# Kernel optimization log

Hardware: AMD Instinct MI355X
Metric: run time of the kernel (lower is better)

Reference implementation:

```python
import jax, jax.numpy as jnp
import numpy as np

SLOPE = 0.01  # torch LeakyReLU default negative_slope

def lrelu(x):
    return jax.nn.leaky_relu(x, SLOPE)

def rgcn_conv(x, edge_index, edge_type, rel_w, root_w, bias, num_relations=2):
    # PyG RGCNConv: out = x @ root + bias + sum_r mean_{edges of rel r into i}(x_j @ W_r)
    N = x.shape[0]
    src, dst = edge_index[0], edge_index[1]
    out = x @ root_w + bias
    # transform once per relation at node level, then gather per edge
    h = jnp.einsum('nd,rde->rne', x, rel_w)          # [R, N, d]
    msg = h[edge_type, src]                           # [E, d] single gather
    for r in range(num_relations):
        m = (edge_type == r)
        s = jax.ops.segment_sum(jnp.where(m[:, None], msg, 0.0), dst, num_segments=N)
        cnt = jax.ops.segment_sum(m.astype(x.dtype), dst, num_segments=N)
        out = out + s / jnp.maximum(cnt, 1.0)[:, None]  # mean aggregation (0 if no edges)
    return out


def setup_inputs() -> dict:
    key = jax.random.key(0)
    ks = jax.random.split(key, 24)
    N, E, H = 50000, 800000, 256
    Q = H // 4
    def lin(k, i, o):
        k1, k2 = jax.random.split(k)
        s = 1.0 / np.sqrt(i)
        return (jax.random.uniform(k1, (i, o), jnp.float32, -s, s),
                jax.random.uniform(k2, (o,), jnp.float32, -s, s))
    Wd, bd = lin(ks[0], 768, Q)
    Wt, bt = lin(ks[1], 768, Q)
    Wn, bn = lin(ks[2], 5, Q)
    Wc, bc = lin(ks[3], 3, Q)
    Wi, bi = lin(ks[4], H, H)
    Wo1, bo1 = lin(ks[5], H, H)
    Wo2, bo2 = lin(ks[6], H, 2)
    s = 1.0 / np.sqrt(H)
    rel_w1 = jax.random.uniform(ks[7], (2, H, H), jnp.float32, -s, s)
    root_w1 = jax.random.uniform(ks[8], (H, H), jnp.float32, -s, s)
    bias1 = jnp.zeros((H,), jnp.float32)
    rel_w2 = jax.random.uniform(ks[9], (2, H, H), jnp.float32, -s, s)
    root_w2 = jax.random.uniform(ks[10], (H, H), jnp.float32, -s, s)
    bias2 = jnp.zeros((H,), jnp.float32)
    return {
        'des': jax.random.normal(ks[11], (N, 768), jnp.float32),
        'tweet': jax.random.normal(ks[12], (N, 768), jnp.float32),
        'num_prop': jax.random.normal(ks[13], (N, 5), jnp.float32),
        'cat_prop': jax.random.normal(ks[14], (N, 3), jnp.float32),
        'edge_index': jax.random.randint(ks[15], (2, E), 0, N, jnp.int32),
        'edge_type': jax.random.randint(ks[16], (E,), 0, 2, jnp.int32),
        'Wd': Wd, 'bd': bd, 'Wt': Wt, 'bt': bt, 'Wn': Wn, 'bn': bn, 'Wc': Wc, 'bc': bc,
        'Wi': Wi, 'bi': bi,
        'rel_w1': rel_w1, 'root_w1': root_w1, 'bias1': bias1,
        'rel_w2': rel_w2, 'root_w2': root_w2, 'bias2': bias2,
        'Wo1': Wo1, 'bo1': bo1, 'Wo2': Wo2, 'bo2': bo2,
    }


def reference(des, tweet, num_prop, cat_prop, edge_index, edge_type,
              Wd, bd, Wt, bt, Wn, bn, Wc, bc, Wi, bi,
              rel_w1, root_w1, bias1, rel_w2, root_w2, bias2,
              Wo1, bo1, Wo2, bo2):
    # dropout is identity in eval mode
    d = lrelu(des @ Wd + bd)
    t = lrelu(tweet @ Wt + bt)
    n = lrelu(num_prop @ Wn + bn)
    c = lrelu(cat_prop @ Wc + bc)
    x = jnp.concatenate([d, t, n, c], axis=1)           # [N, H]
    x = lrelu(x @ Wi + bi)
    x = rgcn_conv(x, edge_index, edge_type, rel_w1, root_w1, bias1)
    x = rgcn_conv(x, edge_index, edge_type, rel_w2, root_w2, bias2)
    x = lrelu(x @ Wo1 + bo1)
    return x @ Wo2 + bo2                                 # [N, 2]
```

## Files before the change

### kernel.cpp

```cpp
#include <hip/hip_runtime.h>
#include <stdint.h>

__device__ __forceinline__ float bf2f(unsigned short h) {
    union { unsigned int u; float f; } x;
    x.u = ((unsigned int)h) << 16;
    return x.f;
}
__device__ __forceinline__ unsigned short f2bf(float f) {
    union { float f; unsigned int u; } x;
    x.f = f;
    unsigned int u = x.u;
    unsigned int r = (u + 0x7FFFu + ((u >> 16) & 1u)) >> 16;
    return (unsigned short)r;
}
__device__ __forceinline__ unsigned pk2(float a, float b) {
    unsigned ua = __float_as_uint(a) + 0x8000u;
    unsigned ub = __float_as_uint(b) + 0x8000u;
    return __builtin_amdgcn_perm(ub, ua, 0x07060302);
}

typedef __attribute__((ext_vector_type(8))) short short8;
typedef __attribute__((ext_vector_type(4))) float floatx4;

__global__ __launch_bounds__(512) void k_encode(
    const float* __restrict__ Ades, const float* __restrict__ Atw,
    const unsigned short* __restrict__ BtDes, const unsigned short* __restrict__ BtTw,
    const unsigned short* __restrict__ bias_bf,
    unsigned short* __restrict__ C, int M)
{
    __shared__ unsigned short Bs[64 * 392];
    const int set = blockIdx.y;
    const float* A = set ? Atw : Ades;
    const unsigned short* Bt = set ? BtTw : BtDes;
    const unsigned short* bias = bias_bf + set * 64;
    const int colofs = set * 64;
    const int tid  = threadIdx.x;
    const int wave = tid >> 6, lane = tid & 63;
    const int quad = lane >> 4, l16 = lane & 15;
    const int ngroups = (M + 15) >> 4;

    const int g0 = blockIdx.x * 8 + wave;
    const int g1 = g0 + (int)(gridDim.x * 8);
    const bool h1 = g1 < ngroups;
    int r0 = g0 * 16 + l16; if (r0 > M - 1) r0 = M - 1;
    int r1g = h1 ? g1 * 16 + l16 : r0; if (r1g > M - 1) r1g = M - 1;

    floatx4 acc0[4], acc1[4];
#pragma unroll
    for (int t = 0; t < 4; t++) {
        acc0[t] = (floatx4){0.f, 0.f, 0.f, 0.f};
        acc1[t] = (floatx4){0.f, 0.f, 0.f, 0.f};
    }

    const bool act0 = g0 < ngroups;

#pragma unroll
    for (int h = 0; h < 2; h++) {
        if (h) __syncthreads();
        for (int c = tid; c < 3072; c += 512) {
            int n = c / 48, kc = (c - n * 48) * 8;
            *(uint4*)&Bs[n * 392 + kc] = ((const uint4*)Bt)[n * 96 + h * 48 + (c - n * 48)];
        }
        __syncthreads();
        if (!act0) continue;

        const float* a0 = A + (size_t)r0 * 768 + h * 384 + quad * 8;
        const float* a1 = A + (size_t)r1g * 768 + h * 384 + quad * 8;
        float4 c0a = *(const float4*)(a0);
        float4 c0b = *(const float4*)(a0 + 4);
        float4 c1a = *(const float4*)(a1);
        float4 c1b = *(const float4*)(a1 + 4);
        float4 n0a = *(const float4*)(a0 + 32);
        float4 n0b = *(const float4*)(a0 + 36);
        float4 n1a = *(const float4*)(a1 + 32);
        float4 n1b = *(const float4*)(a1 + 36);

        for (int s = 0; s < 12; s++) {
            short8 af0, af1;
            unsigned* u0 = (unsigned*)&af0;
            unsigned* u1 = (unsigned*)&af1;
            u0[0] = pk2(c0a.x, c0a.y); u0[1] = pk2(c0a.z, c0a.w);
            u0[2] = pk2(c0b.x, c0b.y); u0[3] = pk2(c0b.z, c0b.w);
            u1[0] = pk2(c1a.x, c1a.y); u1[1] = pk2(c1a.z, c1a.w);
            u1[2] = pk2(c1b.x, c1b.y); u1[3] = pk2(c1b.z, c1b.w);
            c0a = n0a; c0b = n0b; c1a = n1a; c1b = n1b;
            if (s < 10) {
                n0a = *(const float4*)(a0 + (s + 2) * 32);
                n0b = *(const float4*)(a0 + (s + 2) * 32 + 4);
                n1a = *(const float4*)(a1 + (s + 2) * 32);
                n1b = *(const float4*)(a1 + (s + 2) * 32 + 4);
            }
            int kb = s * 32 + quad * 8;
#pragma unroll
            for (int t = 0; t < 4; t++) {
                short8 bfr = *(const short8*)&Bs[(t * 16 + l16) * 392 + kb];
                acc0[t] = __builtin_amdgcn_mfma_f32_16x16x32_bf16(af0, bfr, acc0[t], 0, 0, 0);
                acc1[t] = __builtin_amdgcn_mfma_f32_16x16x32_bf16(af1, bfr, acc1[t], 0, 0, 0);
            }
        }
    }

    if (act0) {
#pragma unroll
        for (int t = 0; t < 4; t++) {
            float bv = bf2f(bias[t * 16 + l16]);
#pragma unroll
            for (int r = 0; r < 4; r++) {
                int row = g0 * 16 + quad * 4 + r;
                if (row < M) {
                    float v = acc0[t][r] + bv;
                    v = v > 0.f ? v : 0.01f * v;
                    C[(size_t)row * 256 + colofs + t * 16 + l16] = f2bf(v);
                }
                if (h1) {
                    int rw = g1 * 16 + quad * 4 + r;
                    if (rw < M) {
                        float v = acc1[t][r] + bv;
                        v = v > 0.f ? v : 0.01f * v;
                        C[(size_t)rw * 256 + colofs + t * 16 + l16] = f2bf(v);
                    }
                }
            }
        }
    }
}

__global__ __launch_bounds__(256) void gemm_nt(
    const unsigned short* __restrict__ A0, const unsigned short* __restrict__ A1,
    const unsigned short* __restrict__ A2, int lda,
    const unsigned short* __restrict__ Bt, int ldb,
    unsigned short* __restrict__ C, int ldc,
    const unsigned short* __restrict__ bias,
    int M, int K, int act)
{
    constexpr int BM = 128, BN = 128, BK = 64;
    const int tid  = threadIdx.x;
    const int wave = tid >> 6;
    const int lane = tid & 63;
    const int quad = lane >> 4;
    const int l16  = lane & 15;
    const int m0   = blockIdx.x * BM;
    const int n0   = blockIdx.y * BN;
    const int wm   = (wave & 1) * 64;
    const int wn   = (wave >> 1) * 64;

    __shared__ short8 As[8 * (BM + 2)];
    __shared__ short8 Bs[8 * (BN + 2)];

    floatx4 acc[4][4];
#pragma unroll
    for (int i = 0; i < 4; i++)
#pragma unroll
        for (int j = 0; j < 4; j++) acc[i][j] = (floatx4){0.f, 0.f, 0.f, 0.f};

    for (int kt = 0; kt < K; kt += BK) {
        const unsigned short* Ap = (kt < 256) ? A0 : (kt < 512) ? A1 : A2;
        const int ko = kt & 255;
#pragma unroll
        for (int c = 0; c < 4; c++) {
            int lin = c * 256 + tid;
            int row = lin >> 3, kq = lin & 7;
            int gr = m0 + row; if (gr > M - 1) gr = M - 1;
            As[kq * (BM + 2) + row] = *(const short8*)(Ap + (size_t)gr * lda + ko + kq * 8);
        }
#pragma unroll
        for (int c = 0; c < 4; c++) {
            int lin = c * 256 + tid;
            int n = lin >> 3, kq = lin & 7;
            Bs[kq * (BN + 2) + n] = *(const short8*)(Bt + (size_t)(n0 + n) * ldb + kt + kq * 8);
        }
        __syncthreads();
#pragma unroll
        for (int s = 0; s < 2; s++) {
            short8 af[4], bfr[4];
#pragma unroll
            for (int i = 0; i < 4; i++)
                af[i] = As[(s * 4 + quad) * (BM + 2) + wm + i * 16 + l16];
#pragma unroll
            for (int j = 0; j < 4; j++)
                bfr[j] = Bs[(s * 4 + quad) * (BN + 2) + wn + j * 16 + l16];
#pragma unroll
            for (int i = 0; i < 4; i++)
#pragma unroll
                for (int j = 0; j < 4; j++)
                    acc[i][j] = __builtin_amdgcn_mfma_f32_16x16x32_bf16(
                        af[i], bfr[j], acc[i][j], 0, 0, 0);
        }
        __syncthreads();
    }

#pragma unroll
    for (int j = 0; j < 4; j++) {
        int gc = n0 + wn + j * 16 + l16;
        float bv = bias ? bf2f(bias[gc]) : 0.f;
#pragma unroll
        for (int i = 0; i < 4; i++) {
            int grb = m0 + wm + i * 16 + quad * 4;
#pragma unroll
            for (int r = 0; r < 4; r++) {
                int gr = grb + r;
                if (gr < M) {
                    float v = acc[i][j][r] + bv;
                    if (act) v = v > 0.f ? v : 0.01f * v;
                    C[(size_t)gr * ldc + gc] = f2bf(v);
                }
            }
        }
    }
}

__global__ void k_prep(const float* __restrict__ Wd, const float* __restrict__ Wt,
                       const float* __restrict__ Wi, const float* __restrict__ Wo1,
                       const float* __restrict__ root1, const float* __restrict__ rel1,
                       const float* __restrict__ root2, const float* __restrict__ rel2,
                       const float* __restrict__ bd, const float* __restrict__ bt,
                       const float* __restrict__ bi, const float* __restrict__ b1,
                       const float* __restrict__ b2, const float* __restrict__ bo1,
                       unsigned short* __restrict__ WdT, unsigned short* __restrict__ WtT,
                       unsigned short* __restrict__ WiT, unsigned short* __restrict__ Wo1T,
                       unsigned short* __restrict__ BT1, unsigned short* __restrict__ BT2,
                       unsigned short* __restrict__ bias_bf)
{
    int i = blockIdx.x * 256 + threadIdx.x;
    if (i < 49152) { int r = i >> 6, c = i & 63; WdT[c * 768 + r] = f2bf(Wd[i]); return; }
    i -= 49152;
    if (i < 49152) { int r = i >> 6, c = i & 63; WtT[c * 768 + r] = f2bf(Wt[i]); return; }
    i -= 49152;
    if (i < 65536) { int r = i >> 8, c = i & 255; WiT[c * 256 + r] = f2bf(Wi[i]); return; }
    i -= 65536;
    if (i < 65536) { int r = i >> 8, c = i & 255; Wo1T[c * 256 + r] = f2bf(Wo1[i]); return; }
    i -= 65536;
    if (i < 196608) {
        int k = i % 768, n = i / 768;
        BT1[i] = f2bf(k < 256 ? root1[k * 256 + n] : rel1[(k - 256) * 256 + n]);
        return;
    }
    i -= 196608;
    if (i < 196608) {
        int k = i % 768, n = i / 768;
        BT2[i] = f2bf(k < 256 ? root2[k * 256 + n] : rel2[(k - 256) * 256 + n]);
        return;
    }
    i -= 196608;
    if (i < 1152) {
        const float* p; int off;
        if (i < 64)       { p = bd;  off = i; }
        else if (i < 128) { p = bt;  off = i - 64; }
        else if (i < 384) { p = bi;  off = i - 128; }
        else if (i < 640) { p = b1;  off = i - 384; }
        else if (i < 896) { p = b2;  off = i - 640; }
        else              { p = bo1; off = i - 896; }
        bias_bf[i] = f2bf(p[off]);
    }
}

__global__ void k_hist(const int* __restrict__ ei, const int* __restrict__ et,
                       int* cnt2, int N, int E) {
    int e = blockIdx.x * 256 + threadIdx.x;
    if (e < E) {
        int dst = ei[E + e];
        int t = et[e] & 1;
        if ((unsigned)dst < (unsigned)N) atomicAdd(&cnt2[t * N + dst], 1);
    }
}

__global__ void k_scan1(const int* __restrict__ cnt2, int* rowptr, int* bsum, int N) {
    __shared__ int sh[256];
    int t = threadIdx.x;
    int base = blockIdx.x * 1024 + t * 4;
    int v[4];
    int s = 0;
#pragma unroll
    for (int k = 0; k < 4; k++) {
        int idx = base + k;
        v[k] = (idx < N) ? (cnt2[idx] + cnt2[N + idx]) : 0;
        s += v[k];
    }
    sh[t] = s;
    __syncthreads();
    for (int off = 1; off < 256; off <<= 1) {
        int x = 0;
        if (t >= off) x = sh[t - off];
        __syncthreads();
        if (t >= off) sh[t] += x;
        __syncthreads();
    }
    int excl = sh[t] - s;
    int run = excl;
#pragma unroll
    for (int k = 0; k < 4; k++) {
        int idx = base + k;
        if (idx < N) rowptr[idx] = run;
        run += v[k];
    }
    if (t == 255) bsum[blockIdx.x] = sh[255];
}

__global__ void k_scan2(const int* __restrict__ bsum, int* bofs, int nb) {
    int t = threadIdx.x;
    int v = (t < nb) ? bsum[t] : 0;
    int orig = v;
    for (int off = 1; off < 64; off <<= 1) {
        int x = __shfl_up(v, off);
        if (t >= off) v += x;
    }
    if (t < nb) bofs[t] = v - orig;
}

__global__ void k_scan3(int* rowptr, const int* __restrict__ bofs, int N) {
    int i = blockIdx.x * 256 + threadIdx.x;
    if (i < N) rowptr[i] += bofs[i >> 10];
}

__global__ void k_fill(const int* __restrict__ ei, const int* __restrict__ et,
                       const int* __restrict__ rowptr, int* cursor, int* sorted,
                       int N, int E) {
    int e = blockIdx.x * 256 + threadIdx.x;
    if (e < E) {
        int src = ei[e];
        int dst = ei[E + e];
        int t = et[e] & 1;
        if ((unsigned)dst < (unsigned)N && (unsigned)src < (unsigned)N) {
            int pos = rowptr[dst] + atomicAdd(&cursor[dst], 1);
            sorted[pos] = src | (t << 24);
        }
    }
}

__global__ __launch_bounds__(256) void k_agg(
    const unsigned short* __restrict__ x,
    unsigned short* __restrict__ m0,
    unsigned short* __restrict__ m1,
    int N,
    const int* __restrict__ rowptr, const int* __restrict__ cnt2,
    const int* __restrict__ sorted)
{
    int wave = threadIdx.x >> 6;
    int lane = threadIdx.x & 63;
    int half = lane >> 5;
    int l32  = lane & 31;
    int node = blockIdx.x * 4 + wave;
    if (node >= N) return;

    int start = rowptr[node];
    int c0 = cnt2[node], c1 = cnt2[N + node];
    int deg = c0 + c1;

    float a0[8] = {0,0,0,0,0,0,0,0};
    float a1[8] = {0,0,0,0,0,0,0,0};

    for (int b = 0; b < deg; b += 64) {
        int rem = deg - b; if (rem > 64) rem = 64;
        int p = 0;
        if (lane < rem) p = sorted[start + b + lane];
        int iters = (rem + 1) >> 1;
        for (int t = 0; t < iters; t += 2) {
            int e0 = 2 * t + half;
            int e1 = e0 + 2;
            int q0 = __shfl(p, e0 < 64 ? e0 : 63);
            int q1 = __shfl(p, e1 < 64 ? e1 : 63);
            bool v0ok = e0 < rem;
            bool v1ok = e1 < rem;
            int s0 = q0 & 0xFFFFFF; if (s0 >= N) s0 = 0;
            int s1 = q1 & 0xFFFFFF; if (s1 >= N) s1 = 0;
            uint4 r0 = *((const uint4*)(x + (size_t)s0 * 256) + l32);
            uint4 r1 = *((const uint4*)(x + (size_t)s1 * 256) + l32);
            if (v0ok) {
                float f[8];
                f[0] = bf2f((unsigned short)(r0.x & 0xFFFFu)); f[1] = bf2f((unsigned short)(r0.x >> 16));
                f[2] = bf2f((unsigned short)(r0.y & 0xFFFFu)); f[3] = bf2f((unsigned short)(r0.y >> 16));
                f[4] = bf2f((unsigned short)(r0.z & 0xFFFFu)); f[5] = bf2f((unsigned short)(r0.z >> 16));
                f[6] = bf2f((unsigned short)(r0.w & 0xFFFFu)); f[7] = bf2f((unsigned short)(r0.w >> 16));
                if ((q0 >> 24) & 1) {
#pragma unroll
                    for (int k = 0; k < 8; k++) a1[k] += f[k];
                } else {
#pragma unroll
                    for (int k = 0; k < 8; k++) a0[k] += f[k];
                }
            }
            if (v1ok) {
                float f[8];
                f[0] = bf2f((unsigned short)(r1.x & 0xFFFFu)); f[1] = bf2f((unsigned short)(r1.x >> 16));
                f[2] = bf2f((unsigned short)(r1.y & 0xFFFFu)); f[3] = bf2f((unsigned short)(r1.y >> 16));
                f[4] = bf2f((unsigned short)(r1.z & 0xFFFFu)); f[5] = bf2f((unsigned short)(r1.z >> 16));
                f[6] = bf2f((unsigned short)(r1.w & 0xFFFFu)); f[7] = bf2f((unsigned short)(r1.w >> 16));
                if ((q1 >> 24) & 1) {
#pragma unroll
                    for (int k = 0; k < 8; k++) a1[k] += f[k];
                } else {
#pragma unroll
                    for (int k = 0; k < 8; k++) a0[k] += f[k];
                }
            }
        }
    }
#pragma unroll
    for (int k = 0; k < 8; k++) {
        a0[k] += __shfl_xor(a0[k], 32);
        a1[k] += __shfl_xor(a1[k], 32);
    }
    float i0 = c0 > 0 ? 1.f / (float)c0 : 0.f;
    float i1 = c1 > 0 ? 1.f / (float)c1 : 0.f;
    uint4 o;
    if (half == 0) {
        o.x = (unsigned)f2bf(a0[0] * i0) | ((unsigned)f2bf(a0[1] * i0) << 16);
        o.y = (unsigned)f2bf(a0[2] * i0) | ((unsigned)f2bf(a0[3] * i0) << 16);
        o.z = (unsigned)f2bf(a0[4] * i0) | ((unsigned)f2bf(a0[5] * i0) << 16);
        o.w = (unsigned)f2bf(a0[6] * i0) | ((unsigned)f2bf(a0[7] * i0) << 16);
        *((uint4*)(m0 + (size_t)node * 256) + l32) = o;
    } else {
        o.x = (unsigned)f2bf(a1[0] * i1) | ((unsigned)f2bf(a1[1] * i1) << 16);
        o.y = (unsigned)f2bf(a1[2] * i1) | ((unsigned)f2bf(a1[3] * i1) << 16);
        o.z = (unsigned)f2bf(a1[4] * i1) | ((unsigned)f2bf(a1[5] * i1) << 16);
        o.w = (unsigned)f2bf(a1[6] * i1) | ((unsigned)f2bf(a1[7] * i1) << 16);
        *((uint4*)(m1 + (size_t)node * 256) + l32) = o;
    }
}

__global__ void k_small(const float* __restrict__ num, const float* __restrict__ cat,
                        const float* __restrict__ Wn, const float* __restrict__ bnp,
                        const float* __restrict__ Wc, const float* __restrict__ bcp,
                        unsigned short* __restrict__ xcat, int N)
{
    __shared__ float wn[320], wc[192], bns[64], bcs[64];
    int t = threadIdx.x;
    for (int i = t; i < 320; i += 256) wn[i] = Wn[i];
    for (int i = t; i < 192; i += 256) wc[i] = Wc[i];
    if (t < 64) { bns[t] = bnp[t]; bcs[t] = bcp[t]; }
    __syncthreads();

    int node = blockIdx.x * 128 + (t >> 1);
    int half = t & 1;
    if (node >= N) return;
    if (half == 0) {
        float in5[5];
#pragma unroll
        for (int i = 0; i < 5; i++) in5[i] = num[(size_t)node * 5 + i];
        unsigned short* orow = xcat + (size_t)node * 256 + 128;
#pragma unroll 4
        for (int c = 0; c < 64; c++) {
            float v = bns[c];
#pragma unroll
            for (int i = 0; i < 5; i++) v += in5[i] * wn[i * 64 + c];
            v = v > 0.f ? v : 0.01f * v;
            orow[c] = f2bf(v);
        }
    } else {
        float in3[3];
#pragma unroll
        for (int i = 0; i < 3; i++) in3[i] = cat[(size_t)node * 3 + i];
        unsigned short* orow = xcat + (size_t)node * 256 + 192;
#pragma unroll 4
        for (int c = 0; c < 64; c++) {
            float v = bcs[c];
#pragma unroll
            for (int i = 0; i < 3; i++) v += in3[i] * wc[i * 64 + c];
            v = v > 0.f ? v : 0.01f * v;
            orow[c] = f2bf(v);
        }
    }
}

__global__ __launch_bounds__(256) void k_final(
    const unsigned short* __restrict__ z,
    const float* __restrict__ Wo2, const float* __restrict__ bo2,
    float* __restrict__ out, int N)
{
    __shared__ float w[512];
    int t = threadIdx.x;
    for (int i = t; i < 512; i += 256) w[i] = Wo2[i];
    __syncthreads();
    int wave = t >> 6, lane = t & 63;
    int node = blockIdx.x * 4 + wave;
    if (node >= N) return;
    uint2 raw = *((const uint2*)(z + (size_t)node * 256) + lane);
    float v0 = bf2f((unsigned short)(raw.x & 0xFFFFu));
    float v1 = bf2f((unsigned short)(raw.x >> 16));
    float v2 = bf2f((unsigned short)(raw.y & 0xFFFFu));
    float v3 = bf2f((unsigned short)(raw.y >> 16));
    int k0 = lane * 4;
    float s0 = v0 * w[k0 * 2]     + v1 * w[(k0 + 1) * 2]     + v2 * w[(k0 + 2) * 2]     + v3 * w[(k0 + 3) * 2];
    float s1 = v0 * w[k0 * 2 + 1] + v1 * w[(k0 + 1) * 2 + 1] + v2 * w[(k0 + 2) * 2 + 1] + v3 * w[(k0 + 3) * 2 + 1];
    for (int off = 32; off; off >>= 1) {
        s0 += __shfl_xor(s0, off);
        s1 += __shfl_xor(s1, off);
    }
    if (lane == 0) {
        out[(size_t)node * 2]     = s0 + bo2[0];
        out[(size_t)node * 2 + 1] = s1 + bo2[1];
    }
}

extern "C" void kernel_launch(void* const* d_in, const int* in_sizes, int n_in,
                              void* d_out, int out_size, void* d_ws, size_t ws_size,
                              hipStream_t stream)
{
    (void)n_in; (void)out_size; (void)ws_size;
    const float* des   = (const float*)d_in[0];
    const float* tweet = (const float*)d_in[1];
    const float* nump  = (const float*)d_in[2];
    const float* catp  = (const float*)d_in[3];
    const int*   ei    = (const int*)d_in[4];
    const int*   et    = (const int*)d_in[5];
    const float* Wd  = (const float*)d_in[6];
    const float* bd  = (const float*)d_in[7];
    const float* Wt  = (const float*)d_in[8];
    const float* bt  = (const float*)d_in[9];
    const float* Wn  = (const float*)d_in[10];
    const float* bn  = (const float*)d_in[11];
    const float* Wc  = (const float*)d_in[12];
    const float* bc  = (const float*)d_in[13];
    const float* Wi  = (const float*)d_in[14];
    const float* bi  = (const float*)d_in[15];
    const float* rel1  = (const float*)d_in[16];
    const float* root1 = (const float*)d_in[17];
    const float* bias1 = (const float*)d_in[18];
    const float* rel2  = (const float*)d_in[19];
    const float* root2 = (const float*)d_in[20];
    const float* bias2 = (const float*)d_in[21];
    const float* Wo1 = (const float*)d_in[22];
    const float* bo1 = (const float*)d_in[23];
    const float* Wo2 = (const float*)d_in[24];
    const float* bo2 = (const float*)d_in[25];

    const int N = in_sizes[0] / 768;
    const int E = in_sizes[5];

    char* ws = (char*)d_ws;
    size_t off = 0;
    auto alloc = [&](size_t bytes) -> char* {
        char* p = ws + off;
        off += (bytes + 255) & ~(size_t)255;
        return p;
    };
    unsigned short* B0 = (unsigned short*)alloc((size_t)N * 256 * 2);
    unsigned short* B1 = (unsigned short*)alloc((size_t)N * 256 * 2);
    unsigned short* B2 = (unsigned short*)alloc((size_t)N * 256 * 2);
    unsigned short* B3 = (unsigned short*)alloc((size_t)N * 256 * 2);
    unsigned short* WdT  = (unsigned short*)alloc(64 * 768 * 2);
    unsigned short* WtT  = (unsigned short*)alloc(64 * 768 * 2);
    unsigned short* WiT  = (unsigned short*)alloc(256 * 256 * 2);
    unsigned short* Wo1T = (unsigned short*)alloc(256 * 256 * 2);
    unsigned short* BT1  = (unsigned short*)alloc(256 * 768 * 2);
    unsigned short* BT2  = (unsigned short*)alloc(256 * 768 * 2);
    unsigned short* bias_bf = (unsigned short*)alloc(1152 * 2);
    unsigned short* bd_bf = bias_bf;
    unsigned short* bi_bf = bias_bf + 128;
    unsigned short* b1_bf = bias_bf + 384;
    unsigned short* b2_bf = bias_bf + 640;
    unsigned short* bo1_bf = bias_bf + 896;
    int* cnt2   = (int*)alloc((size_t)2 * N * 4);
    int* cursor = (int*)alloc((size_t)N * 4);
    int* rowptr = (int*)alloc((size_t)(N + 1) * 4);
    int* bsum   = (int*)alloc(64 * 4);
    int* bofs   = (int*)alloc(64 * 4);
    int* sorted = (int*)alloc((size_t)E * 4);

    size_t zlen = (size_t)(((char*)cursor + (size_t)N * 4) - (char*)cnt2);
    hipMemsetAsync(cnt2, 0, zlen, stream);

    k_prep<<<(623744 + 255) / 256, 256, 0, stream>>>(
        Wd, Wt, Wi, Wo1, root1, rel1, root2, rel2,
        bd, bt, bi, bias1, bias2, bo1,
        WdT, WtT, WiT, Wo1T, BT1, BT2, bias_bf);

    int eb = (E + 255) / 256;
    k_hist<<<eb, 256, 0, stream>>>(ei, et, cnt2, N, E);
    int nb = (N + 1023) / 1024;
    k_scan1<<<nb, 256, 0, stream>>>(cnt2, rowptr, bsum, N);
    k_scan2<<<1, 64, 0, stream>>>(bsum, bofs, nb);
    k_scan3<<<(N + 255) / 256, 256, 0, stream>>>(rowptr, bofs, N);
    k_fill<<<eb, 256, 0, stream>>>(ei, et, rowptr, cursor, sorted, N, E);

    dim3 gEnc(256, 2);
    k_encode<<<gEnc, 512, 0, stream>>>(des, tweet, WdT, WtT, bd_bf, B0, N);
    k_small<<<(N + 127) / 128, 256, 0, stream>>>(nump, catp, Wn, bn, Wc, bc, B0, N);

    dim3 g128((N + 127) / 128, 2);
    gemm_nt<<<g128, 256, 0, stream>>>(B0, B0, B0, 256, WiT, 256, B1, 256, bi_bf, N, 256, 1);

    int ab = (N + 3) / 4;
    k_agg<<<ab, 256, 0, stream>>>(B1, B2, B3, N, rowptr, cnt2, sorted);
    gemm_nt<<<g128, 256, 0, stream>>>(B1, B2, B3, 256, BT1, 768, B0, 256, b1_bf, N, 768, 0);

    k_agg<<<ab, 256, 0, stream>>>(B0, B2, B3, N, rowptr, cnt2, sorted);
    gemm_nt<<<g128, 256, 0, stream>>>(B0, B2, B3, 256, BT2, 768, B1, 256, b2_bf, N, 768, 0);

    gemm_nt<<<g128, 256, 0, stream>>>(B1, B1, B1, 256, Wo1T, 256, B0, 256, bo1_bf, N, 256, 1);

    k_final<<<ab, 256, 0, stream>>>(B0, Wo2, bo2, (float*)d_out, N);
}
```

Baseline: 750.6 us.

## Restructure encoder GEMM into 64-row tiles with swizzled LDS staging of A and B

The encoder kernel used to give each wave two 16-row groups, read fp32 A directly from global memory per lane, and keep half of the weight matrix in a padded shared buffer. It now launches one 256-thread block per 64 rows and stages both A (converted to bf16) and B through small XOR-swizzled shared tiles in 64-wide K steps. This aims to coalesce the A loads, shrink LDS use for higher occupancy, and avoid bank conflicts. In exchange it adds a sync per K step with no double buffering and reloads the weights in every block.

```diff
diff --git a/kernel.cpp b/kernel.cpp
--- a/kernel.cpp
+++ b/kernel.cpp
@@ -22,104 +22,79 @@
 typedef __attribute__((ext_vector_type(8))) short short8;
 typedef __attribute__((ext_vector_type(4))) float floatx4;
 
-__global__ __launch_bounds__(512) void k_encode(
+__global__ __launch_bounds__(256) void k_encode(
     const float* __restrict__ Ades, const float* __restrict__ Atw,
     const unsigned short* __restrict__ BtDes, const unsigned short* __restrict__ BtTw,
     const unsigned short* __restrict__ bias_bf,
     unsigned short* __restrict__ C, int M)
 {
-    __shared__ unsigned short Bs[64 * 392];
+    __shared__ __align__(16) unsigned short Asw[64 * 64];
+    __shared__ __align__(16) unsigned short Bsw[64 * 64];
+
     const int set = blockIdx.y;
     const float* A = set ? Atw : Ades;
     const unsigned short* Bt = set ? BtTw : BtDes;
     const unsigned short* bias = bias_bf + set * 64;
     const int colofs = set * 64;
     const int tid  = threadIdx.x;
-    const int wave = tid >> 6, lane = tid & 63;
+    const int wv   = tid >> 6, lane = tid & 63;
     const int quad = lane >> 4, l16 = lane & 15;
-    const int ngroups = (M + 15) >> 4;
-
-    const int g0 = blockIdx.x * 8 + wave;
-    const int g1 = g0 + (int)(gridDim.x * 8);
-    const bool h1 = g1 < ngroups;
-    int r0 = g0 * 16 + l16; if (r0 > M - 1) r0 = M - 1;
-    int r1g = h1 ? g1 * 16 + l16 : r0; if (r1g > M - 1) r1g = M - 1;
-
-    floatx4 acc0[4], acc1[4];
-#pragma unroll
-    for (int t = 0; t < 4; t++) {
-        acc0[t] = (floatx4){0.f, 0.f, 0.f, 0.f};
-        acc1[t] = (floatx4){0.f, 0.f, 0.f, 0.f};
-    }
-
-    const bool act0 = g0 < ngroups;
-
-#pragma unroll
-    for (int h = 0; h < 2; h++) {
-        if (h) __syncthreads();
-        for (int c = tid; c < 3072; c += 512) {
-            int n = c / 48, kc = (c - n * 48) * 8;
-            *(uint4*)&Bs[n * 392 + kc] = ((const uint4*)Bt)[n * 96 + h * 48 + (c - n * 48)];
+    const int m0   = blockIdx.x * 64;
+
+    const int ar  = tid >> 4;
+    const int af4 = tid & 15;
+    const int bcol = tid >> 3;
+    const int bq   = tid & 7;
+
+    floatx4 acc[4];
+#pragma unroll
+    for (int j = 0; j < 4; j++) acc[j] = (floatx4){0.f, 0.f, 0.f, 0.f};
+
+    for (int kt = 0; kt < 768; kt += 64) {
+        if (kt) __syncthreads();
+#pragma unroll
+        for (int p = 0; p < 4; p++) {
+            int row = p * 16 + ar;
+            int gr = m0 + row; if (gr > M - 1) gr = M - 1;
+            float4 v = *(const float4*)(A + (size_t)gr * 768 + kt + af4 * 4);
+            unsigned w0 = pk2(v.x, v.y), w1 = pk2(v.z, v.w);
+            int qd = (af4 >> 1) ^ (row & 7);
+            uint2 u; u.x = w0; u.y = w1;
+            *(uint2*)&Asw[row * 64 + qd * 8 + (af4 & 1) * 4] = u;
+        }
+#pragma unroll
+        for (int p = 0; p < 2; p++) {
+            int col = p * 32 + bcol;
+            short8 bv = *(const short8*)(Bt + (size_t)col * 768 + kt + bq * 8);
+            int qd = bq ^ (col & 7);
+            *(short8*)&Bsw[col * 64 + qd * 8] = bv;
         }
         __syncthreads();
-        if (!act0) continue;
-
-        const float* a0 = A + (size_t)r0 * 768 + h * 384 + quad * 8;
-        const float* a1 = A + (size_t)r1g * 768 + h * 384 + quad * 8;
-        float4 c0a = *(const float4*)(a0);
-        float4 c0b = *(const float4*)(a0 + 4);
-        float4 c1a = *(const float4*)(a1);
-        float4 c1b = *(const float4*)(a1 + 4);
-        float4 n0a = *(const float4*)(a0 + 32);
-        float4 n0b = *(const float4*)(a0 + 36);
-        float4 n1a = *(const float4*)(a1 + 32);
-        float4 n1b = *(const float4*)(a1 + 36);
-
-        for (int s = 0; s < 12; s++) {
-            short8 af0, af1;
-            unsigned* u0 = (unsigned*)&af0;
-            unsigned* u1 = (unsigned*)&af1;
-            u0[0] = pk2(c0a.x, c0a.y); u0[1] = pk2(c0a.z, c0a.w);
-            u0[2] = pk2(c0b.x, c0b.y); u0[3] = pk2(c0b.z, c0b.w);
-            u1[0] = pk2(c1a.x, c1a.y); u1[1] = pk2(c1a.z, c1a.w);
-            u1[2] = pk2(c1b.x, c1b.y); u1[3] = pk2(c1b.z, c1b.w);
-            c0a = n0a; c0b = n0b; c1a = n1a; c1b = n1b;
-            if (s < 10) {
-                n0a = *(const float4*)(a0 + (s + 2) * 32);
-                n0b = *(const float4*)(a0 + (s + 2) * 32 + 4);
-                n1a = *(const float4*)(a1 + (s + 2) * 32);
-                n1b = *(const float4*)(a1 + (s + 2) * 32 + 4);
+#pragma unroll
+        for (int s = 0; s < 2; s++) {
+            int arow = wv * 16 + l16;
+            int ca = (s * 4 + quad) ^ (arow & 7);
+            short8 av = *(const short8*)&Asw[arow * 64 + ca * 8];
+#pragma unroll
+            for (int j = 0; j < 4; j++) {
+                int bcl = j * 16 + l16;
+                int cb = (s * 4 + quad) ^ (bcl & 7);
+                short8 bvr = *(const short8*)&Bsw[bcl * 64 + cb * 8];
+                acc[j] = __builtin_amdgcn_mfma_f32_16x16x32_bf16(av, bvr, acc[j], 0, 0, 0);
             }
-            int kb = s * 32 + quad * 8;
-#pragma unroll
-            for (int t = 0; t < 4; t++) {
-                short8 bfr = *(const short8*)&Bs[(t * 16 + l16) * 392 + kb];
-                acc0[t] = __builtin_amdgcn_mfma_f32_16x16x32_bf16(af0, bfr, acc0[t], 0, 0, 0);
-                acc1[t] = __builtin_amdgcn_mfma_f32_16x16x32_bf16(af1, bfr, acc1[t], 0, 0, 0);
-            }
-        }
-    }
-
-    if (act0) {
-#pragma unroll
-        for (int t = 0; t < 4; t++) {
-            float bv = bf2f(bias[t * 16 + l16]);
-#pragma unroll
-            for (int r = 0; r < 4; r++) {
-                int row = g0 * 16 + quad * 4 + r;
-                if (row < M) {
-                    float v = acc0[t][r] + bv;
-                    v = v > 0.f ? v : 0.01f * v;
-                    C[(size_t)row * 256 + colofs + t * 16 + l16] = f2bf(v);
-                }
-                if (h1) {
-                    int rw = g1 * 16 + quad * 4 + r;
-                    if (rw < M) {
-                        float v = acc1[t][r] + bv;
-                        v = v > 0.f ? v : 0.01f * v;
-                        C[(size_t)rw * 256 + colofs + t * 16 + l16] = f2bf(v);
-                    }
-                }
+        }
+    }
+
+#pragma unroll
+    for (int j = 0; j < 4; j++) {
+        float bv = bf2f(bias[j * 16 + l16]);
+#pragma unroll
+        for (int r = 0; r < 4; r++) {
+            int gr = m0 + wv * 16 + quad * 4 + r;
+            if (gr < M) {
+                float v = acc[j][r] + bv;
+                v = v > 0.f ? v : 0.01f * v;
+                C[(size_t)gr * 256 + colofs + j * 16 + l16] = f2bf(v);
             }
         }
     }
@@ -573,8 +548,8 @@
     k_scan3<<<(N + 255) / 256, 256, 0, stream>>>(rowptr, bofs, N);
     k_fill<<<eb, 256, 0, stream>>>(ei, et, rowptr, cursor, sorted, N, E);
 
-    dim3 gEnc(256, 2);
-    k_encode<<<gEnc, 512, 0, stream>>>(des, tweet, WdT, WtT, bd_bf, B0, N);
+    dim3 gEnc((N + 63) / 64, 2);
+    k_encode<<<gEnc, 256, 0, stream>>>(des, tweet, WdT, WtT, bd_bf, B0, N);
     k_small<<<(N + 127) / 128, 256, 0, stream>>>(nump, catp, Wn, bn, Wc, bc, B0, N);
 
     dim3 g128((N + 127) / 128, 2);
```

Result: no change. 743.9 us (-0.9%).
